# Kernel optimization log

Hardware: AMD Instinct MI355X
Metric: run time of the kernel (lower is better)

## Reference

```python
import jax, jax.numpy as jnp
import numpy as np

NEG_INF = float('-inf')

def setup_inputs() -> dict:
    key = jax.random.key(0)
    k1, k2 = jax.random.split(key)
    B, T, S, H, D = 2, 2048, 2048, 8, 64
    q = jax.random.normal(k1, (B, T, H, D), dtype=jnp.float32)
    kv = jax.random.normal(k2, (B, S, 2, H, D), dtype=jnp.float32)
    key_padding_mask = jnp.ones((B, S), dtype=bool)  # True = valid key
    return {"q": q, "kv": kv, "key_padding_mask": key_padding_mask, "causal": 1}


def reference(q, kv, key_padding_mask, causal):
    # q: (B,T,H,D), kv: (B,S,2,H,D)
    k = kv[:, :, 0]  # (B,S,H,D)
    v = kv[:, :, 1]  # (B,S,H,D)
    D = q.shape[-1]
    scale = D ** (-0.5)
    # scores: (B,H,T,S)
    scores = jnp.einsum('bthd,bshd->bhts', q, k) * scale
    # mask: True means "mask out" (matches torch masked_fill semantics)
    mask = ~key_padding_mask[:, None, None, :]  # (B,1,1,S)
    if causal:
        T, S = scores.shape[2], scores.shape[3]
        causal_mask = jnp.triu(jnp.ones((T, S), dtype=bool), k=1)  # (T,S)
        mask = mask | causal_mask[None, None, :, :]
    scores = jnp.where(mask, NEG_INF, scores)
    attn = jax.nn.softmax(scores, axis=-1)
    out = jnp.einsum('bhts,bshd->bthd', attn, v)  # (B,T,H,D)
    return out
```

## Files before the change

kernel.cpp:

```cpp
#include <hip/hip_runtime.h>
#include <hip/hip_bf16.h>

typedef __bf16 bf8_t __attribute__((ext_vector_type(8)));
typedef float  f4_t  __attribute__((ext_vector_type(4)));
typedef int    i4_t  __attribute__((ext_vector_type(4)));

constexpr int Bc = 2;
constexpr int Tc = 2048;
constexpr int Sc = 2048;
constexpr int Hc = 8;
constexpr int Dc = 64;
constexpr int BQ = 64;
constexpr int BK = 32;
constexpr int nQB = Tc / BQ;
constexpr int NKT = Sc / BK;
constexpr int NP  = nQB / 2;
constexpr int NS  = 4;
constexpr int TILE_H = 4096;
constexpr int KH = 2048;
constexpr int SLOT_H = 8192;

__device__ __forceinline__ void g2l16(const void* g, void* l) {
    __builtin_amdgcn_global_load_lds(
        (const __attribute__((address_space(1))) void*)g,
        (__attribute__((address_space(3))) void*)l, 16, 0, 0);
}

__device__ __forceinline__ int pack_bf16(float lo, float hi) {
    const unsigned l16 = (unsigned)__builtin_bit_cast(unsigned short, (__bf16)lo);
    const unsigned h16 = (unsigned)__builtin_bit_cast(unsigned short, (__bf16)hi);
    return (int)(l16 | (h16 << 16));
}

__global__ __launch_bounds__(256)
void fa_prep(const float* __restrict__ kv, const int* __restrict__ kpm,
             __bf16* __restrict__ kvb, unsigned* __restrict__ kpmw)
{
    const int idx    = blockIdx.x * 256 + threadIdx.x;
    const int tile   = idx >> 9;
    const int within = idx & 511;
    const int b  = tile >> 9;
    const int h  = (tile >> 6) & 7;
    const int s0 = (tile & 63) * BK;
    bf8_t o;
    __bf16* dst;
    if (within < 256) {
        const int row = within >> 3;
        const int col = ((within & 7) * 8) ^ ((row & 7) << 3);
        const float* src = kv + (((size_t)(b * Sc + s0 + row) * 2 + 0) * Hc + h) * Dc + col;
        const float4 x0 = *(const float4*)src;
        const float4 x1 = *(const float4*)(src + 4);
        o[0] = (__bf16)x0.x; o[1] = (__bf16)x0.y; o[2] = (__bf16)x0.z; o[3] = (__bf16)x0.w;
        o[4] = (__bf16)x1.x; o[5] = (__bf16)x1.y; o[6] = (__bf16)x1.z; o[7] = (__bf16)x1.w;
        dst = kvb + (size_t)tile * TILE_H + within * 8;
    } else {
        const int c    = within - 256;
        const int vrow = c >> 2;
        const int g8   = c & 3;
        const float* src = kv + (((size_t)(b * Sc + s0 + g8 * 8) * 2 + 1) * Hc + h) * Dc + vrow;
        #pragma unroll
        for (int j = 0; j < 8; ++j) o[j] = (__bf16)src[(size_t)j * 2 * Hc * Dc];
        const int r  = vrow >> 1;
        const int gg = ((vrow & 1) * 4 + g8) ^ (r & 7);
        dst = kvb + (size_t)tile * TILE_H + KH + r * 64 + gg * 8;
    }
    *(bf8_t*)dst = o;

    if (idx < Bc * NKT) {
        const int bb = idx >> 6, tt = idx & 63;
        unsigned m = 0;
        for (int k = 0; k < 32; ++k)
            m |= (kpm[bb * Sc + tt * BK + k] != 0 ? 1u : 0u) << k;
        kpmw[idx] = m;
    }
}

__global__ __launch_bounds__(256, 4)
void fa_part(const float* __restrict__ q,
             const __bf16* __restrict__ kvb,
             const unsigned* __restrict__ kpmw,
             const int* __restrict__ causal_p,
             float* __restrict__ part_o,
             float* __restrict__ part_l)
{
    __shared__ __bf16 shKV[2 * SLOT_H];

    const int tid  = threadIdx.x;
    const int wave = tid >> 6;
    const int lane = tid & 63;
    const int n16  = lane & 15;
    const int quad = lane >> 4;

    const int bid = blockIdx.x;
    const int h   = bid & 7;
    const int g   = bid >> 3;
    const int b   = g / (NP * NS);
    const int rem = g % (NP * NS);
    const int p   = rem / NS;
    const int s   = rem % NS;
    const int causal = causal_p[0];

    const int nA   = causal ? (nQB - p)  : 32;
    const int nB   = causal ? (p + 1)    : 32;
    const int ntot = nA + nB;
    const int lo   = (ntot * s + NS - 1) / NS;
    const int hi   = (ntot * (s + 1) + NS - 1) / NS;

    const __bf16* kvt = kvb + (size_t)((b * Hc + h) * NKT) * TILE_H;
    const unsigned* mw_b = kpmw + b * NKT;

    const int kA_off = n16 * 64 + ((quad * 8) ^ ((n16 & 7) << 3));
    const int vRd    = (n16 >> 1) * 64 +
                       ((((n16 & 1) << 2) | quad) ^ (n16 >> 1)) * 8;
    const int lds_st = tid * 8;
    const int addrA  = (n16 + ((quad & 1) << 5)) << 2;
    const int addrB  = addrA + 64;
    const bool hiQ   = quad >= 2;
    const float scale = 0.125f;

    #pragma unroll 1
    for (int seg = 0; seg < 2; ++seg) {
        const int qt = seg ? p : (nQB - 1 - p);
        const int t0 = seg ? (max(lo, nA) - nA) : lo;
        const int t1 = seg ? (hi - nA)          : min(hi, nA);
        if (t0 >= t1) continue;

        __syncthreads();

        const int q_base = qt * BQ;
        const int tqn    = q_base + wave * 16 + n16;

        bf8_t a_q[2];
        {
            const float* qrow = q + ((size_t)(b * Tc + tqn) * Hc + h) * Dc;
            #pragma unroll
            for (int f = 0; f < 2; ++f) {
                const float4 x0 = *(const float4*)(qrow + f * 32 + quad * 8);
                const float4 x1 = *(const float4*)(qrow + f * 32 + quad * 8 + 4);
                bf8_t v;
                v[0] = (__bf16)(x0.x * scale); v[1] = (__bf16)(x0.y * scale);
                v[2] = (__bf16)(x0.z * scale); v[3] = (__bf16)(x0.w * scale);
                v[4] = (__bf16)(x1.x * scale); v[5] = (__bf16)(x1.y * scale);
                v[6] = (__bf16)(x1.z * scale); v[7] = (__bf16)(x1.w * scale);
                a_q[f] = v;
            }
        }

        f4_t o_acc[4];
        #pragma unroll
        for (int dt = 0; dt < 4; ++dt) o_acc[dt] = (f4_t){0.f, 0.f, 0.f, 0.f};
        float lsum = 0.f;

        int cu = 0;
        {
            const __bf16* src = kvt + (size_t)(2 * t0) * TILE_H;
            g2l16(src + lds_st,               &shKV[lds_st]);
            g2l16(src + TILE_H + lds_st,      &shKV[2048 + lds_st]);
            g2l16(src + KH + lds_st,          &shKV[4096 + lds_st]);
            g2l16(src + TILE_H + KH + lds_st, &shKV[6144 + lds_st]);
        }

        for (int it = t0; it < t1; ++it) {
            const int kb = it * 64;
            const unsigned cm0 = mw_b[2 * it];
            const unsigned cm1 = mw_b[2 * it + 1];
            const int nx = cu ^ SLOT_H;

            if (it + 1 < t1) {
                const __bf16* srcn = kvt + (size_t)(2 * (it + 1)) * TILE_H;
                g2l16(srcn + lds_st,               &shKV[nx + lds_st]);
                g2l16(srcn + TILE_H + lds_st,      &shKV[nx + 2048 + lds_st]);
                g2l16(srcn + KH + lds_st,          &shKV[nx + 4096 + lds_st]);
                g2l16(srcn + TILE_H + KH + lds_st, &shKV[nx + 6144 + lds_st]);
                asm volatile("s_waitcnt vmcnt(4)" ::: "memory");
            } else {
                asm volatile("s_waitcnt vmcnt(0)" ::: "memory");
            }
            __builtin_amdgcn_s_barrier();

            #pragma unroll
            for (int hh = 0; hh < 2; ++hh) {
                const unsigned cmw = hh ? cm1 : cm0;
                int pk[2][2];
                #pragma unroll
                for (int sub = 0; sub < 2; ++sub) {
                    const int kbase = cu + hh * 2048 + sub * 1024;
                    const bf8_t bk0 = *(const bf8_t*)&shKV[kbase + kA_off];
                    const bf8_t bk1 = *(const bf8_t*)&shKV[kbase + (kA_off ^ 32)];
                    f4_t acc = (f4_t){0.f, 0.f, 0.f, 0.f};
                    __builtin_amdgcn_s_setprio(1);
                    acc = __builtin_amdgcn_mfma_f32_16x16x32_bf16(bk0, a_q[0], acc, 0, 0, 0);
                    acc = __builtin_amdgcn_mfma_f32_16x16x32_bf16(bk1, a_q[1], acc, 0, 0, 0);
                    __builtin_amdgcn_s_setprio(0);
                    const int keyb = kb + hh * 32 + sub * 16 + quad * 4;
                    const unsigned mb = cmw >> (sub * 16 + quad * 4);
                    float pv[4];
                    #pragma unroll
                    for (int r = 0; r < 4; ++r) {
                        const bool valid = ((mb >> r) & 1u) && (!causal || keyb + r <= tqn);
                        const float pp = valid ? __expf(acc[r] - 8.0f) : 0.0f;
                        lsum += pp;
                        pv[r] = pp;
                    }
                    pk[sub][0] = pack_bf16(pv[0], pv[1]);
                    pk[sub][1] = pack_bf16(pv[2], pv[3]);
                }

                const int a0 = __builtin_amdgcn_ds_bpermute(addrA, pk[0][0]);
                const int a1 = __builtin_amdgcn_ds_bpermute(addrA, pk[0][1]);
                const int b0 = __builtin_amdgcn_ds_bpermute(addrB, pk[0][0]);
                const int b1 = __builtin_amdgcn_ds_bpermute(addrB, pk[0][1]);
                const int c0 = __builtin_amdgcn_ds_bpermute(addrA, pk[1][0]);
                const int c1 = __builtin_amdgcn_ds_bpermute(addrA, pk[1][1]);
                const int d0 = __builtin_amdgcn_ds_bpermute(addrB, pk[1][0]);
                const int d1 = __builtin_amdgcn_ds_bpermute(addrB, pk[1][1]);
                union { i4_t i; bf8_t b; } u;
                u.i[0] = hiQ ? c0 : a0;
                u.i[1] = hiQ ? c1 : a1;
                u.i[2] = hiQ ? d0 : b0;
                u.i[3] = hiQ ? d1 : b1;
                const bf8_t a_p = u.b;

                const int vb = cu + 4096 + hh * 2048 + vRd;
                const bf8_t bv0 = *(const bf8_t*)&shKV[vb];
                const bf8_t bv1 = *(const bf8_t*)&shKV[vb + 512];
                const bf8_t bv2 = *(const bf8_t*)&shKV[vb + 1024];
                const bf8_t bv3 = *(const bf8_t*)&shKV[vb + 1536];
                __builtin_amdgcn_s_setprio(1);
                o_acc[0] = __builtin_amdgcn_mfma_f32_16x16x32_bf16(a_p, bv0, o_acc[0], 0, 0, 0);
                o_acc[1] = __builtin_amdgcn_mfma_f32_16x16x32_bf16(a_p, bv1, o_acc[1], 0, 0, 0);
                o_acc[2] = __builtin_amdgcn_mfma_f32_16x16x32_bf16(a_p, bv2, o_acc[2], 0, 0, 0);
                o_acc[3] = __builtin_amdgcn_mfma_f32_16x16x32_bf16(a_p, bv3, o_acc[3], 0, 0, 0);
                __builtin_amdgcn_s_setprio(0);
            }

            __builtin_amdgcn_s_barrier();
            cu = nx;
        }

        lsum += __shfl_xor(lsum, 16);
        lsum += __shfl_xor(lsum, 32);
        float l_row[4];
        #pragma unroll
        for (int r = 0; r < 4; ++r) {
            const int li = __builtin_amdgcn_ds_bpermute((quad * 4 + r) << 2,
                                                        __builtin_bit_cast(int, lsum));
            l_row[r] = __builtin_bit_cast(float, li);
        }

        const size_t slot = (size_t)(((b * Hc + h) * NP + p) * NS + s) * 2 + seg;
        float* po = part_o + slot * (BQ * Dc);
        #pragma unroll
        for (int dt = 0; dt < 4; ++dt) {
            #pragma unroll
            for (int r = 0; r < 4; ++r) {
                const int row = wave * 16 + quad * 4 + r;
                po[row * Dc + dt * 16 + n16] = o_acc[dt][r];
            }
        }
        if (n16 == 0) {
            #pragma unroll
            for (int r = 0; r < 4; ++r) {
                const int row = wave * 16 + quad * 4 + r;
                part_l[slot * BQ + row] = l_row[r];
            }
        }
    }
}

__global__ __launch_bounds__(256, 4)
void fa_reduce(const float* __restrict__ part_o,
               const float* __restrict__ part_l,
               const int* __restrict__ causal_p,
               float* __restrict__ out)
{
    const int gtid = blockIdx.x * 256 + threadIdx.x;
    const int e    = gtid & (BQ * Dc / 4 - 1);
    const int qi   = gtid >> 10;
    const int row  = e >> 4;
    const int d4   = e & 15;

    const int qt = qi & (nQB - 1);
    const int h  = (qi >> 5) & (Hc - 1);
    const int b  = qi >> 8;
    const int causal = causal_p[0];

    const int p    = (qt < NP) ? qt : (nQB - 1 - qt);
    const int seg  = (qt < NP) ? 1 : 0;
    const int nA   = causal ? (nQB - p) : 32;
    const int nB   = causal ? (p + 1)   : 32;
    const int ntot = nA + nB;
    const int segLo = seg ? nA : 0;
    const int segHi = seg ? ntot : nA;

    float4 acc = make_float4(0.f, 0.f, 0.f, 0.f);
    float  l   = 0.f;
    #pragma unroll
    for (int s = 0; s < NS; ++s) {
        const int lo = (ntot * s + NS - 1) / NS;
        const int hi = (ntot * (s + 1) + NS - 1) / NS;
        if (lo < segHi && segLo < hi && lo < hi) {
            const size_t slot = (size_t)(((b * Hc + h) * NP + p) * NS + s) * 2 + seg;
            const float4 v = *(const float4*)(part_o + slot * (BQ * Dc) + row * Dc + d4 * 4);
            acc.x += v.x; acc.y += v.y; acc.z += v.z; acc.w += v.w;
            l += part_l[slot * BQ + row];
        }
    }
    const float inv = 1.0f / l;
    const int t = qt * BQ + row;
    float4 o;
    o.x = acc.x * inv; o.y = acc.y * inv; o.z = acc.z * inv; o.w = acc.w * inv;
    *(float4*)(out + ((size_t)(b * Tc + t) * Hc + h) * Dc + d4 * 4) = o;
}

extern "C" void kernel_launch(void* const* d_in, const int* in_sizes, int n_in,
                              void* d_out, int out_size, void* d_ws, size_t ws_size,
                              hipStream_t stream) {
    const float* q   = (const float*)d_in[0];
    const float* kv  = (const float*)d_in[1];
    const int*   kpm = (const int*)d_in[2];
    const int*   cz  = (const int*)d_in[3];
    float*       out = (float*)d_out;

    __bf16* kvb = (__bf16*)d_ws;
    const size_t kvb_bytes = (size_t)Bc * Hc * NKT * TILE_H * sizeof(__bf16);
    unsigned* kpmw = (unsigned*)((char*)d_ws + kvb_bytes);
    float* part_o  = (float*)((char*)d_ws + kvb_bytes + 4096);

    const size_t nslots = (size_t)Bc * Hc * NP * NS * 2;
    float* part_l = part_o + nslots * (BQ * Dc);

    const int grid0 = Bc * Hc * NKT * 512 / 256;
    fa_prep<<<grid0, 256, 0, stream>>>(kv, kpm, kvb, kpmw);

    const int grid1 = Bc * Hc * NP * NS;
    fa_part<<<grid1, 256, 0, stream>>>(q, kvb, kpmw, cz, part_o, part_l);

    const int grid2 = (int)((size_t)Bc * Hc * nQB * (BQ * Dc / 4) / 256);
    fa_reduce<<<grid2, 256, 0, stream>>>(part_o, part_l, cz, out);
}
```

Baseline: 112.0 us.

## Double query tile to 128 rows with 8 waves sharing each K/V tile

Raises the query block from 64 to 128 rows and launches 512 threads, so each K/V tile loaded into LDS is reused by twice as many waves. The causal tile counts and the reduce indexing are recomputed for the new tile size. The load schedule changes to one wait plus one barrier per iteration, with the next tile's mask words prefetched alongside it, and the MFMA priority hints are removed. The trade-off is half as many blocks in the grid and twice as many threads per block, which lowers the number of concurrent blocks and may leave load imbalance across the causal pairs.

```diff
diff --git a/kernel.cpp b/kernel.cpp
--- a/kernel.cpp
+++ b/kernel.cpp
@@ -10,7 +10,7 @@
 constexpr int Sc = 2048;
 constexpr int Hc = 8;
 constexpr int Dc = 64;
-constexpr int BQ = 64;
+constexpr int BQ = 128;
 constexpr int BK = 32;
 constexpr int nQB = Tc / BQ;
 constexpr int NKT = Sc / BK;
@@ -75,7 +75,7 @@
     }
 }
 
-__global__ __launch_bounds__(256, 4)
+__global__ __launch_bounds__(512, 4)
 void fa_part(const float* __restrict__ q,
              const __bf16* __restrict__ kvb,
              const unsigned* __restrict__ kpmw,
@@ -100,8 +100,8 @@
     const int s   = rem % NS;
     const int causal = causal_p[0];
 
-    const int nA   = causal ? (nQB - p)  : 32;
-    const int nB   = causal ? (p + 1)    : 32;
+    const int nA   = causal ? (32 - 2 * p) : 32;
+    const int nB   = causal ? (2 * p + 2)  : 32;
     const int ntot = nA + nB;
     const int lo   = (ntot * s + NS - 1) / NS;
     const int hi   = (ntot * (s + 1) + NS - 1) / NS;
@@ -112,7 +112,12 @@
     const int kA_off = n16 * 64 + ((quad * 8) ^ ((n16 & 7) << 3));
     const int vRd    = (n16 >> 1) * 64 +
                        ((((n16 & 1) << 2) | quad) ^ (n16 >> 1)) * 8;
-    const int lds_st = tid * 8;
+    const int img    = tid >> 8;
+    const int c8     = (tid & 255) * 8;
+    const int srcK   = img * TILE_H + c8;
+    const int srcV   = img * TILE_H + KH + c8;
+    const int ldsK   = img * 2048 + c8;
+    const int ldsV   = 4096 + img * 2048 + c8;
     const int addrA  = (n16 + ((quad & 1) << 5)) << 2;
     const int addrB  = addrA + 64;
     const bool hiQ   = quad >= 2;
@@ -152,32 +157,30 @@
         float lsum = 0.f;
 
         int cu = 0;
+        unsigned cm0, cm1;
         {
             const __bf16* src = kvt + (size_t)(2 * t0) * TILE_H;
-            g2l16(src + lds_st,               &shKV[lds_st]);
-            g2l16(src + TILE_H + lds_st,      &shKV[2048 + lds_st]);
-            g2l16(src + KH + lds_st,          &shKV[4096 + lds_st]);
-            g2l16(src + TILE_H + KH + lds_st, &shKV[6144 + lds_st]);
+            g2l16(src + srcK, &shKV[ldsK]);
+            g2l16(src + srcV, &shKV[ldsV]);
+            cm0 = mw_b[2 * t0];
+            cm1 = mw_b[2 * t0 + 1];
         }
 
         for (int it = t0; it < t1; ++it) {
-            const int kb = it * 64;
-            const unsigned cm0 = mw_b[2 * it];
-            const unsigned cm1 = mw_b[2 * it + 1];
+            asm volatile("s_waitcnt vmcnt(0)" ::: "memory");
+            __builtin_amdgcn_s_barrier();
+
             const int nx = cu ^ SLOT_H;
-
+            unsigned nm0 = 0, nm1 = 0;
             if (it + 1 < t1) {
                 const __bf16* srcn = kvt + (size_t)(2 * (it + 1)) * TILE_H;
-                g2l16(srcn + lds_st,               &shKV[nx + lds_st]);
-                g2l16(srcn + TILE_H + lds_st,      &shKV[nx + 2048 + lds_st]);
-                g2l16(srcn + KH + lds_st,          &shKV[nx + 4096 + lds_st]);
-                g2l16(srcn + TILE_H + KH + lds_st, &shKV[nx + 6144 + lds_st]);
-                asm volatile("s_waitcnt vmcnt(4)" ::: "memory");
-            } else {
-                asm volatile("s_waitcnt vmcnt(0)" ::: "memory");
-            }
-            __builtin_amdgcn_s_barrier();
-
+                g2l16(srcn + srcK, &shKV[nx + ldsK]);
+                g2l16(srcn + srcV, &shKV[nx + ldsV]);
+                nm0 = mw_b[2 * it + 2];
+                nm1 = mw_b[2 * it + 3];
+            }
+
+            const int kb = it * 64;
             #pragma unroll
             for (int hh = 0; hh < 2; ++hh) {
                 const unsigned cmw = hh ? cm1 : cm0;
@@ -188,10 +191,8 @@
                     const bf8_t bk0 = *(const bf8_t*)&shKV[kbase + kA_off];
                     const bf8_t bk1 = *(const bf8_t*)&shKV[kbase + (kA_off ^ 32)];
                     f4_t acc = (f4_t){0.f, 0.f, 0.f, 0.f};
-                    __builtin_amdgcn_s_setprio(1);
                     acc = __builtin_amdgcn_mfma_f32_16x16x32_bf16(bk0, a_q[0], acc, 0, 0, 0);
                     acc = __builtin_amdgcn_mfma_f32_16x16x32_bf16(bk1, a_q[1], acc, 0, 0, 0);
-                    __builtin_amdgcn_s_setprio(0);
                     const int keyb = kb + hh * 32 + sub * 16 + quad * 4;
                     const unsigned mb = cmw >> (sub * 16 + quad * 4);
                     float pv[4];
@@ -226,16 +227,13 @@
                 const bf8_t bv1 = *(const bf8_t*)&shKV[vb + 512];
                 const bf8_t bv2 = *(const bf8_t*)&shKV[vb + 1024];
                 const bf8_t bv3 = *(const bf8_t*)&shKV[vb + 1536];
-                __builtin_amdgcn_s_setprio(1);
                 o_acc[0] = __builtin_amdgcn_mfma_f32_16x16x32_bf16(a_p, bv0, o_acc[0], 0, 0, 0);
                 o_acc[1] = __builtin_amdgcn_mfma_f32_16x16x32_bf16(a_p, bv1, o_acc[1], 0, 0, 0);
                 o_acc[2] = __builtin_amdgcn_mfma_f32_16x16x32_bf16(a_p, bv2, o_acc[2], 0, 0, 0);
                 o_acc[3] = __builtin_amdgcn_mfma_f32_16x16x32_bf16(a_p, bv3, o_acc[3], 0, 0, 0);
-                __builtin_amdgcn_s_setprio(0);
-            }
-
-            __builtin_amdgcn_s_barrier();
-            cu = nx;
+            }
+
+            cm0 = nm0; cm1 = nm1; cu = nx;
         }
 
         lsum += __shfl_xor(lsum, 16);
@@ -276,19 +274,19 @@
 {
     const int gtid = blockIdx.x * 256 + threadIdx.x;
     const int e    = gtid & (BQ * Dc / 4 - 1);
-    const int qi   = gtid >> 10;
+    const int qi   = gtid >> 11;
     const int row  = e >> 4;
     const int d4   = e & 15;
 
     const int qt = qi & (nQB - 1);
-    const int h  = (qi >> 5) & (Hc - 1);
-    const int b  = qi >> 8;
+    const int h  = (qi >> 4) & (Hc - 1);
+    const int b  = qi >> 7;
     const int causal = causal_p[0];
 
     const int p    = (qt < NP) ? qt : (nQB - 1 - qt);
     const int seg  = (qt < NP) ? 1 : 0;
-    const int nA   = causal ? (nQB - p) : 32;
-    const int nB   = causal ? (p + 1)   : 32;
+    const int nA   = causal ? (32 - 2 * p) : 32;
+    const int nB   = causal ? (2 * p + 2)  : 32;
     const int ntot = nA + nB;
     const int segLo = seg ? nA : 0;
     const int segHi = seg ? ntot : nA;
@@ -334,7 +332,7 @@
     fa_prep<<<grid0, 256, 0, stream>>>(kv, kpm, kvb, kpmw);
 
     const int grid1 = Bc * Hc * NP * NS;
-    fa_part<<<grid1, 256, 0, stream>>>(q, kvb, kpmw, cz, part_o, part_l);
+    fa_part<<<grid1, 512, 0, stream>>>(q, kvb, kpmw, cz, part_o, part_l);
 
     const int grid2 = (int)((size_t)Bc * Hc * nQB * (BQ * Dc / 4) / 256);
     fa_reduce<<<grid2, 256, 0, stream>>>(part_o, part_l, cz, out);
```

Result: no change. 111.8 us (-0.1%).
